# Kernel optimization log

Hardware: AMD Instinct MI355X
Metric: run time of the kernel (lower is better)

## Reference

```python
import jax, jax.numpy as jnp
import numpy as np

N = 50000      # nodes
E = 800000     # edges
D_IN = 128     # input feature dim
HID = 64       # out_channels (per-head dim; concat=False -> head mean)
HEADS = 2
NEG_SLOPE = 0.2


def gat_layer(x, src, dst, Ws, Wd, a_s, a_d, b):
    # PyG GATConv, add_self_loops=False, concat=False (mean over heads)
    n = x.shape[0]
    H, C = a_s.shape
    hs = (x @ Ws).reshape(n, H, C)          # source-side features [N,H,C]
    hd = (x @ Wd).reshape(n, H, C)          # dest-side features   [N,H,C]
    als = (hs * a_s).sum(-1)                # [N,H]
    ald = (hd * a_d).sum(-1)                # [N,H]
    e = jax.nn.leaky_relu(als[src] + ald[dst], NEG_SLOPE)   # [E,H]
    # segment softmax over edges grouped by destination node
    m = jax.ops.segment_max(e, dst, num_segments=n)
    m = jax.lax.stop_gradient(jnp.where(jnp.isfinite(m), m, 0.0))
    ex = jnp.exp(e - m[dst])
    den = jax.ops.segment_sum(ex, dst, num_segments=n)
    alpha = ex / (den[dst] + 1e-16)                          # [E,H]
    out = jax.ops.segment_sum(hs[src] * alpha[:, :, None], dst, num_segments=n)
    return out.mean(axis=1) + b             # [N,C]


def setup_inputs() -> dict:
    key = jax.random.key(0)
    ks = jax.random.split(key, 32)
    d = {}
    d["x"] = jax.random.normal(ks[0], (N, D_IN), jnp.float32)
    d["edge_index"] = jax.random.randint(ks[1], (2, E), 0, N, jnp.int32)
    dins = [D_IN, HID, HID]
    i = 2
    for l in range(1, 4):
        din = dins[l - 1]
        s = 1.0 / np.sqrt(din)
        d[f"Ws{l}"] = jax.random.normal(ks[i], (din, HEADS * HID), jnp.float32) * s; i += 1
        d[f"Wd{l}"] = jax.random.normal(ks[i], (din, HEADS * HID), jnp.float32) * s; i += 1
        d[f"as{l}"] = jax.random.normal(ks[i], (HEADS, HID), jnp.float32) * 0.1; i += 1
        d[f"ad{l}"] = jax.random.normal(ks[i], (HEADS, HID), jnp.float32) * 0.1; i += 1
        d[f"b{l}"] = jnp.zeros((HID,), jnp.float32)
        d[f"Wl{l}"] = jax.random.normal(ks[i], (din, HID), jnp.float32) * s; i += 1
        d[f"bl{l}"] = jnp.zeros((HID,), jnp.float32)
    return d


def reference(x, edge_index,
              Ws1, Wd1, as1, ad1, b1, Wl1, bl1,
              Ws2, Wd2, as2, ad2, b2, Wl2, bl2,
              Ws3, Wd3, as3, ad3, b3, Wl3, bl3):
    src, dst = edge_index[0], edge_index[1]
    h = jax.nn.relu(gat_layer(x, src, dst, Ws1, Wd1, as1, ad1, b1) + x @ Wl1 + bl1)
    h = jax.nn.relu(gat_layer(h, src, dst, Ws2, Wd2, as2, ad2, b2) + h @ Wl2 + bl2)
    h = jax.nn.relu(gat_layer(h, src, dst, Ws3, Wd3, as3, ad3, b3) + h @ Wl3 + bl3)
    return h
```

## Files before the change

### kernel.cpp

```cpp
#include <hip/hip_runtime.h>
#include <hip/hip_bf16.h>

#define NN 50000
#define NE 800000
#define SCAN_BS 1024
#define SCAN_NB ((NN + SCAN_BS - 1) / SCAN_BS)

typedef __attribute__((ext_vector_type(8))) __bf16 bf16x8;
typedef __attribute__((ext_vector_type(4))) float float4v;

__device__ __forceinline__ unsigned pack_bf2(float lo, float hi) {
    union { __bf16 b; unsigned short u; } a, c;
    a.b = (__bf16)lo; c.b = (__bf16)hi;
    return (unsigned)a.u | ((unsigned)c.u << 16);
}
__device__ __forceinline__ float2 unpack_bf2(unsigned v) {
    union { unsigned short u; __bf16 b; } lo, hi;
    lo.u = (unsigned short)(v & 0xffff); hi.u = (unsigned short)(v >> 16);
    return make_float2((float)lo.b, (float)hi.b);
}


__global__ void __launch_bounds__(256)
hist_kernel(const int* __restrict__ ei, int* __restrict__ deg, int* __restrict__ rank)
{
    int e = blockIdx.x * 256 + threadIdx.x;
    if (e >= NE) return;
    rank[e] = atomicAdd(&deg[ei[NE + e]], 1);
}

__global__ void __launch_bounds__(SCAN_BS)
scan1_kernel(const int* __restrict__ deg, int* __restrict__ exl, int* __restrict__ bsum)
{
    __shared__ int sh[SCAN_BS];
    int t = threadIdx.x;
    int i = blockIdx.x * SCAN_BS + t;
    int v = (i < NN) ? deg[i] : 0;
    sh[t] = v;
    __syncthreads();
    for (int off = 1; off < SCAN_BS; off <<= 1) {
        int u = (t >= off) ? sh[t - off] : 0;
        __syncthreads();
        sh[t] += u;
        __syncthreads();
    }
    if (i < NN) exl[i] = sh[t] - v;
    if (t == SCAN_BS - 1) bsum[blockIdx.x] = sh[t];
}

__global__ void __launch_bounds__(64)
scan2_kernel(const int* __restrict__ bsum, int* __restrict__ boff, int* __restrict__ row)
{
    int l = threadIdx.x;
    int v = (l < SCAN_NB) ? bsum[l] : 0;
    int own = v;
    for (int off = 1; off < 64; off <<= 1) {
        int u = __shfl_up(v, off);
        if (l >= off) v += u;
    }
    if (l < SCAN_NB) boff[l] = v - own;
    if (l == 63) row[NN] = v;
}

__global__ void __launch_bounds__(SCAN_BS)
scan3_kernel(const int* __restrict__ exl, const int* __restrict__ boff,
             int* __restrict__ row)
{
    int i = blockIdx.x * SCAN_BS + threadIdx.x;
    if (i >= NN) return;
    row[i] = exl[i] + boff[blockIdx.x];
}

__global__ void __launch_bounds__(256)
scatter_kernel(const int* __restrict__ ei, const int* __restrict__ rank,
               const int* __restrict__ row, int* __restrict__ csr_src)
{
    int e = blockIdx.x * 256 + threadIdx.x;
    if (e >= NE) return;
    int s = ei[e], d = ei[NE + e];
    int p = row[d] + rank[e];
    csr_src[p] = s;
}


__global__ void __launch_bounds__(256)
convert_x_kernel(const float* __restrict__ x, __bf16* __restrict__ xb, int n)
{
    int i = blockIdx.x * 256 + threadIdx.x;
    if (i < n) xb[i] = (__bf16)x[i];
}

template <int K>
__global__ void __launch_bounds__(256)
convert_w_kernel(const float* __restrict__ Ws, const float* __restrict__ Wd,
                 const float* __restrict__ Wl, __bf16* __restrict__ Wt)
{
    int i = blockIdx.x * 256 + threadIdx.x;
    if (i >= 320 * K) return;
    int c = i / K, k = i % K;
    float v;
    if (c < 128)      v = Ws[k * 128 + c];
    else if (c < 256) v = Wd[k * 128 + (c - 128)];
    else              v = Wl[k * 64 + (c - 256)];
    Wt[i] = (__bf16)v;
}

template <int K>
__global__ void __launch_bounds__(256)
mfma_gemm(const __bf16* __restrict__ xb, const __bf16* __restrict__ Wt,
          const float* __restrict__ a_s, const float* __restrict__ a_d,
          unsigned* __restrict__ hsb, float* __restrict__ lin,
          float* __restrict__ als, float* __restrict__ ald)
{
    __shared__ __align__(16) char ldsW[320 * 144];

    const int tid  = threadIdx.x;
    const int lane = tid & 63;
    const int wave = tid >> 6;
    const int l15 = lane & 15, quad = lane >> 4;
    const int n0 = blockIdx.x * 64 + wave * 16;
    const int nA = min(n0 + l15, NN - 1);

    bf16x8 afr[K / 32];
#pragma unroll
    for (int ks = 0; ks < K / 32; ++ks)
        afr[ks] = *(const bf16x8*)(xb + (size_t)nA * K + ks * 32 + quad * 8);

    float4v acc[20];
#pragma unroll
    for (int t = 0; t < 20; ++t) acc[t] = (float4v){0.f, 0.f, 0.f, 0.f};

#pragma unroll
    for (int h = 0; h < K / 64; ++h) {
        uint4 tmp[10];
#pragma unroll
        for (int i = 0; i < 10; ++i) {
            int idx = i * 256 + tid;
            int r = idx >> 3, c = idx & 7;
            tmp[i] = *(const uint4*)(Wt + (size_t)r * K + h * 64 + c * 8);
        }
        if (h) __syncthreads();
#pragma unroll
        for (int i = 0; i < 10; ++i) {
            int idx = i * 256 + tid;
            int r = idx >> 3, c = idx & 7;
            *(uint4*)&ldsW[r * 144 + c * 16] = tmp[i];
        }
        __syncthreads();

#pragma unroll
        for (int ksh = 0; ksh < 2; ++ksh) {
            int ks = h * 2 + ksh;
#pragma unroll
            for (int t = 0; t < 20; ++t) {
                bf16x8 bf = *(const bf16x8*)&ldsW[(t * 16 + l15) * 144 + (ksh * 4 + quad) * 16];
                acc[t] = __builtin_amdgcn_mfma_f32_16x16x32_bf16(afr[ks], bf, acc[t], 0, 0, 0);
            }
        }
    }

#pragma unroll
    for (int t = 0; t < 4; ++t) {
        int col = t * 16 + l15;
#pragma unroll
        for (int r = 0; r < 4; ++r) {
            int n = n0 + quad * 4 + r;
            if (n < NN) hsb[(size_t)n * 64 + col] = pack_bf2(acc[t][r], acc[t + 4][r]);
        }
    }
#pragma unroll
    for (int t = 16; t < 20; ++t) {
        int col = (t - 16) * 16 + l15;
#pragma unroll
        for (int r = 0; r < 4; ++r) {
            int n = n0 + quad * 4 + r;
            if (n < NN) lin[(size_t)n * 64 + col] = acc[t][r];
        }
    }

    float s0[4], s1[4], d0[4], d1[4];
#pragma unroll
    for (int r = 0; r < 4; ++r) { s0[r] = 0.f; s1[r] = 0.f; d0[r] = 0.f; d1[r] = 0.f; }
#pragma unroll
    for (int t = 0; t < 4; ++t) {
        float as0 = a_s[t * 16 + l15];
        float as1 = a_s[64 + t * 16 + l15];
        float ad0 = a_d[t * 16 + l15];
        float ad1 = a_d[64 + t * 16 + l15];
#pragma unroll
        for (int r = 0; r < 4; ++r) {
            s0[r] += acc[t][r] * as0;
            s1[r] += acc[t + 4][r] * as1;
            d0[r] += acc[t + 8][r] * ad0;
            d1[r] += acc[t + 12][r] * ad1;
        }
    }
#pragma unroll
    for (int m = 1; m < 16; m <<= 1) {
#pragma unroll
        for (int r = 0; r < 4; ++r) {
            s0[r] += __shfl_xor(s0[r], m);
            s1[r] += __shfl_xor(s1[r], m);
            d0[r] += __shfl_xor(d0[r], m);
            d1[r] += __shfl_xor(d1[r], m);
        }
    }
    if (l15 == 0) {
#pragma unroll
        for (int r = 0; r < 4; ++r) {
            int n = n0 + quad * 4 + r;
            if (n < NN) {
                als[n * 2 + 0] = s0[r];
                als[n * 2 + 1] = s1[r];
                ald[n * 2 + 0] = d0[r];
                ald[n * 2 + 1] = d1[r];
            }
        }
    }
}


__device__ __forceinline__ float2 edge_w(const float* __restrict__ als, int s,
                                         float ad0, float ad1)
{
    float2 al = *(const float2*)&als[s * 2];
    float e0 = al.x + ad0; e0 = (e0 >= 0.f) ? e0 : 0.2f * e0;
    float e1 = al.y + ad1; e1 = (e1 >= 0.f) ? e1 : 0.2f * e1;
    return make_float2(__expf(e0), __expf(e1));
}

__device__ __forceinline__ void store_q(float* p, float v0, float v1, float v2, float v3) {
    *(float4*)p = make_float4(v0, v1, v2, v3);
}
__device__ __forceinline__ void store_q(__bf16* p, float v0, float v1, float v2, float v3) {
    *(uint2*)p = make_uint2(pack_bf2(v0, v1), pack_bf2(v2, v3));
}

template <typename TO>
__global__ void __launch_bounds__(256)
gat_aggregate(const int* __restrict__ row, const int* __restrict__ csr_src,
              const float* __restrict__ als, const float* __restrict__ ald,
              const unsigned* __restrict__ hsb, const float* __restrict__ lin,
              const float* __restrict__ b, const float* __restrict__ bl,
              TO* __restrict__ out)
{
    int w = (blockIdx.x * 256 + threadIdx.x) >> 6;
    int lane = threadIdx.x & 63;
    int q = lane >> 4;
    int l15 = lane & 15;
    if (w >= NN) return;
    int p0 = row[w], p1 = row[w + 1];
    float ad0 = ald[w * 2 + 0];
    float ad1 = ald[w * 2 + 1];

    float a0[4] = {0.f, 0.f, 0.f, 0.f};
    float a1[4] = {0.f, 0.f, 0.f, 0.f};
    float den0 = 0.f, den1 = 0.f;

    int p = p0 + q;
    for (; p + 4 < p1; p += 8) {
        int sA = csr_src[p];
        int sB = csr_src[p + 4];
        float2 eA = edge_w(als, sA, ad0, ad1);
        float2 eB = edge_w(als, sB, ad0, ad1);
        uint4 gA = *(const uint4*)&hsb[(size_t)sA * 64 + 4 * l15];
        uint4 gB = *(const uint4*)&hsb[(size_t)sB * 64 + 4 * l15];
        den0 += eA.x + eB.x;
        den1 += eA.y + eB.y;
        float2 h;
        h = unpack_bf2(gA.x); a0[0] += eA.x * h.x; a1[0] += eA.y * h.y;
        h = unpack_bf2(gA.y); a0[1] += eA.x * h.x; a1[1] += eA.y * h.y;
        h = unpack_bf2(gA.z); a0[2] += eA.x * h.x; a1[2] += eA.y * h.y;
        h = unpack_bf2(gA.w); a0[3] += eA.x * h.x; a1[3] += eA.y * h.y;
        h = unpack_bf2(gB.x); a0[0] += eB.x * h.x; a1[0] += eB.y * h.y;
        h = unpack_bf2(gB.y); a0[1] += eB.x * h.x; a1[1] += eB.y * h.y;
        h = unpack_bf2(gB.z); a0[2] += eB.x * h.x; a1[2] += eB.y * h.y;
        h = unpack_bf2(gB.w); a0[3] += eB.x * h.x; a1[3] += eB.y * h.y;
    }
    for (; p < p1; p += 4) {
        int s = csr_src[p];
        float2 e = edge_w(als, s, ad0, ad1);
        uint4 g = *(const uint4*)&hsb[(size_t)s * 64 + 4 * l15];
        den0 += e.x; den1 += e.y;
        float2 h;
        h = unpack_bf2(g.x); a0[0] += e.x * h.x; a1[0] += e.y * h.y;
        h = unpack_bf2(g.y); a0[1] += e.x * h.x; a1[1] += e.y * h.y;
        h = unpack_bf2(g.z); a0[2] += e.x * h.x; a1[2] += e.y * h.y;
        h = unpack_bf2(g.w); a0[3] += e.x * h.x; a1[3] += e.y * h.y;
    }

#pragma unroll
    for (int i = 0; i < 4; ++i) {
        a0[i] += __shfl_xor(a0[i], 16); a0[i] += __shfl_xor(a0[i], 32);
        a1[i] += __shfl_xor(a1[i], 16); a1[i] += __shfl_xor(a1[i], 32);
    }
    den0 += __shfl_xor(den0, 16); den0 += __shfl_xor(den0, 32);
    den1 += __shfl_xor(den1, 16); den1 += __shfl_xor(den1, 32);

    if (q == 0) {
        int c0 = 4 * l15;
        float r0 = 1.f / (den0 + 1e-16f);
        float r1 = 1.f / (den1 + 1e-16f);
        float4 lv = *(const float4*)&lin[(size_t)w * 64 + c0];
        float v0 = 0.5f * (a0[0] * r0 + a1[0] * r1) + b[c0 + 0] + bl[c0 + 0] + lv.x;
        float v1 = 0.5f * (a0[1] * r0 + a1[1] * r1) + b[c0 + 1] + bl[c0 + 1] + lv.y;
        float v2 = 0.5f * (a0[2] * r0 + a1[2] * r1) + b[c0 + 2] + bl[c0 + 2] + lv.z;
        float v3 = 0.5f * (a0[3] * r0 + a1[3] * r1) + b[c0 + 3] + bl[c0 + 3] + lv.w;
        store_q(&out[(size_t)w * 64 + c0],
                fmaxf(v0, 0.f), fmaxf(v1, 0.f), fmaxf(v2, 0.f), fmaxf(v3, 0.f));
    }
}


extern "C" void kernel_launch(void* const* d_in, const int* in_sizes, int n_in,
                              void* d_out, int out_size, void* d_ws, size_t ws_size,
                              hipStream_t stream)
{
    const float* x  = (const float*)d_in[0];
    const int*   ei = (const int*)d_in[1];
    const float* Ws[3]; const float* Wd[3]; const float* As[3]; const float* Ad[3];
    const float* Bb[3]; const float* Wl[3]; const float* Bl[3];
    for (int l = 0; l < 3; ++l) {
        int base = 2 + 7 * l;
        Ws[l] = (const float*)d_in[base + 0];
        Wd[l] = (const float*)d_in[base + 1];
        As[l] = (const float*)d_in[base + 2];
        Ad[l] = (const float*)d_in[base + 3];
        Bb[l] = (const float*)d_in[base + 4];
        Wl[l] = (const float*)d_in[base + 5];
        Bl[l] = (const float*)d_in[base + 6];
    }

    float* ws = (float*)d_ws;
    unsigned* hsb = (unsigned*)ws;
    float* lin  = (float*)(hsb + (size_t)NN * 64);
    float* als  = lin + (size_t)NN * 64;
    float* ald  = als + (size_t)NN * 2;
    __bf16* xb  = (__bf16*)(ald + (size_t)NN * 2);
    __bf16* hb  = xb + (size_t)NN * 128;
    __bf16* Wt1 = hb + (size_t)NN * 64;
    __bf16* Wt2 = Wt1 + 320 * 128;
    __bf16* Wt3 = Wt2 + 320 * 64;
    int* row     = (int*)(Wt3 + 320 * 64);
    int* deg     = row + (NN + 1);
    int* rank    = deg + NN;
    int* exl     = rank + NE;
    int* bsum    = exl + NN;
    int* boff    = bsum + SCAN_NB;
    int* csr_src = boff + SCAN_NB;

    const int EB  = (NE + 255) / 256;
    const int WB  = (NN * 64 + 255) / 256;
    const int GB  = (NN + 63) / 64;

    hipMemsetAsync(deg, 0, sizeof(int) * NN, stream);
    hist_kernel<<<EB, 256, 0, stream>>>(ei, deg, rank);
    scan1_kernel<<<SCAN_NB, SCAN_BS, 0, stream>>>(deg, exl, bsum);
    scan2_kernel<<<1, 64, 0, stream>>>(bsum, boff, row);
    scan3_kernel<<<SCAN_NB, SCAN_BS, 0, stream>>>(exl, boff, row);
    scatter_kernel<<<EB, 256, 0, stream>>>(ei, rank, row, csr_src);

    convert_x_kernel<<<(NN * 128 + 255) / 256, 256, 0, stream>>>(x, xb, NN * 128);
    convert_w_kernel<128><<<(320 * 128 + 255) / 256, 256, 0, stream>>>(Ws[0], Wd[0], Wl[0], Wt1);
    convert_w_kernel<64><<<(320 * 64 + 255) / 256, 256, 0, stream>>>(Ws[1], Wd[1], Wl[1], Wt2);
    convert_w_kernel<64><<<(320 * 64 + 255) / 256, 256, 0, stream>>>(Ws[2], Wd[2], Wl[2], Wt3);

    for (int l = 0; l < 3; ++l) {
        if (l == 0) {
            mfma_gemm<128><<<GB, 256, 0, stream>>>(xb, Wt1, As[0], Ad[0], hsb, lin, als, ald);
        } else {
            const __bf16* wt = (l == 1) ? Wt2 : Wt3;
            mfma_gemm<64><<<GB, 256, 0, stream>>>(hb, wt, As[l], Ad[l], hsb, lin, als, ald);
        }
        if (l == 2) {
            gat_aggregate<float><<<WB, 256, 0, stream>>>(
                row, csr_src, als, ald, hsb, lin, Bb[l], Bl[l], (float*)d_out);
        } else {
            gat_aggregate<__bf16><<<WB, 256, 0, stream>>>(
                row, csr_src, als, ald, hsb, lin, Bb[l], Bl[l], hb);
        }
    }
}
```

Measured before the change: 372.8 us.

## Fuse weight conversion into histogram kernel, convert x in GEMM, unroll aggregation

Merges the three weight-conversion launches into the edge-histogram kernel as extra blocks. The separate fp32-to-bf16 conversion of x is dropped, and the layer-1 GEMM now loads fp32 x and converts it in registers. The aggregation edge loop gets a 4-way unrolled main loop ahead of the existing 2-way loop. Together these cut launches and one full write and read of x, and raise memory-level parallelism in the gather. The costs are a larger first-layer A load (fp32 instead of bf16) and higher register pressure in the aggregation kernel.

Measured after the change: 353.3 us. 5.2% less time.

```diff
diff --git a/kernel.cpp b/kernel.cpp
--- a/kernel.cpp
+++ b/kernel.cpp
@@ -5,6 +5,7 @@
 #define NE 800000
 #define SCAN_BS 1024
 #define SCAN_NB ((NN + SCAN_BS - 1) / SCAN_BS)
+#define EB ((NE + 255) / 256)
 
 typedef __attribute__((ext_vector_type(8))) __bf16 bf16x8;
 typedef __attribute__((ext_vector_type(4))) float float4v;
@@ -21,13 +22,42 @@
 }
 
 
+__device__ __forceinline__ void convert_w_part(const float* __restrict__ Ws,
+                                               const float* __restrict__ Wd,
+                                               const float* __restrict__ Wl,
+                                               __bf16* __restrict__ Wt, int K, int i)
+{
+    if (i >= 320 * K) return;
+    int c = i / K, k = i % K;
+    float v;
+    if (c < 128)      v = Ws[k * 128 + c];
+    else if (c < 256) v = Wd[k * 128 + (c - 128)];
+    else              v = Wl[k * 64 + (c - 256)];
+    Wt[i] = (__bf16)v;
+}
+
 __global__ void __launch_bounds__(256)
-hist_kernel(const int* __restrict__ ei, int* __restrict__ deg, int* __restrict__ rank)
-{
-    int e = blockIdx.x * 256 + threadIdx.x;
-    if (e >= NE) return;
-    rank[e] = atomicAdd(&deg[ei[NE + e]], 1);
-}
+prep_kernel(const int* __restrict__ ei, int* __restrict__ deg, int* __restrict__ rank,
+            const float* __restrict__ Ws1, const float* __restrict__ Wd1,
+            const float* __restrict__ Wl1, __bf16* __restrict__ Wt1,
+            const float* __restrict__ Ws2, const float* __restrict__ Wd2,
+            const float* __restrict__ Wl2, __bf16* __restrict__ Wt2,
+            const float* __restrict__ Ws3, const float* __restrict__ Wd3,
+            const float* __restrict__ Wl3, __bf16* __restrict__ Wt3)
+{
+    int bi = blockIdx.x;
+    if (bi < EB) {
+        int e = bi * 256 + threadIdx.x;
+        if (e < NE) rank[e] = atomicAdd(&deg[ei[NE + e]], 1);
+    } else if (bi < EB + 160) {
+        convert_w_part(Ws1, Wd1, Wl1, Wt1, 128, (bi - EB) * 256 + threadIdx.x);
+    } else if (bi < EB + 240) {
+        convert_w_part(Ws2, Wd2, Wl2, Wt2, 64, (bi - EB - 160) * 256 + threadIdx.x);
+    } else {
+        convert_w_part(Ws3, Wd3, Wl3, Wt3, 64, (bi - EB - 240) * 256 + threadIdx.x);
+    }
+}
+
 
 __global__ void __launch_bounds__(SCAN_BS)
 scan1_kernel(const int* __restrict__ deg, int* __restrict__ exl, int* __restrict__ bsum)
@@ -83,31 +113,19 @@
 }
 
 
+__device__ __forceinline__ bf16x8 load_af(const __bf16* p) { return *(const bf16x8*)p; }
+__device__ __forceinline__ bf16x8 load_af(const float* p) {
+    float4 u = *(const float4*)p;
+    float4 v = *(const float4*)(p + 4);
+    bf16x8 r;
+    r[0] = (__bf16)u.x; r[1] = (__bf16)u.y; r[2] = (__bf16)u.z; r[3] = (__bf16)u.w;
+    r[4] = (__bf16)v.x; r[5] = (__bf16)v.y; r[6] = (__bf16)v.z; r[7] = (__bf16)v.w;
+    return r;
+}
+
+template <int K, typename TIN>
 __global__ void __launch_bounds__(256)
-convert_x_kernel(const float* __restrict__ x, __bf16* __restrict__ xb, int n)
-{
-    int i = blockIdx.x * 256 + threadIdx.x;
-    if (i < n) xb[i] = (__bf16)x[i];
-}
-
-template <int K>
-__global__ void __launch_bounds__(256)
-convert_w_kernel(const float* __restrict__ Ws, const float* __restrict__ Wd,
-                 const float* __restrict__ Wl, __bf16* __restrict__ Wt)
-{
-    int i = blockIdx.x * 256 + threadIdx.x;
-    if (i >= 320 * K) return;
-    int c = i / K, k = i % K;
-    float v;
-    if (c < 128)      v = Ws[k * 128 + c];
-    else if (c < 256) v = Wd[k * 128 + (c - 128)];
-    else              v = Wl[k * 64 + (c - 256)];
-    Wt[i] = (__bf16)v;
-}
-
-template <int K>
-__global__ void __launch_bounds__(256)
-mfma_gemm(const __bf16* __restrict__ xb, const __bf16* __restrict__ Wt,
+mfma_gemm(const TIN* __restrict__ xin, const __bf16* __restrict__ Wt,
           const float* __restrict__ a_s, const float* __restrict__ a_d,
           unsigned* __restrict__ hsb, float* __restrict__ lin,
           float* __restrict__ als, float* __restrict__ ald)
@@ -124,7 +142,7 @@
     bf16x8 afr[K / 32];
 #pragma unroll
     for (int ks = 0; ks < K / 32; ++ks)
-        afr[ks] = *(const bf16x8*)(xb + (size_t)nA * K + ks * 32 + quad * 8);
+        afr[ks] = load_af(xin + (size_t)nA * K + ks * 32 + quad * 8);
 
     float4v acc[20];
 #pragma unroll
@@ -258,6 +276,39 @@
     float den0 = 0.f, den1 = 0.f;
 
     int p = p0 + q;
+    for (; p + 12 < p1; p += 16) {
+        int sA = csr_src[p];
+        int sB = csr_src[p + 4];
+        int sC = csr_src[p + 8];
+        int sD = csr_src[p + 12];
+        float2 eA = edge_w(als, sA, ad0, ad1);
+        float2 eB = edge_w(als, sB, ad0, ad1);
+        float2 eC = edge_w(als, sC, ad0, ad1);
+        float2 eD = edge_w(als, sD, ad0, ad1);
+        uint4 gA = *(const uint4*)&hsb[(size_t)sA * 64 + 4 * l15];
+        uint4 gB = *(const uint4*)&hsb[(size_t)sB * 64 + 4 * l15];
+        uint4 gC = *(const uint4*)&hsb[(size_t)sC * 64 + 4 * l15];
+        uint4 gD = *(const uint4*)&hsb[(size_t)sD * 64 + 4 * l15];
+        den0 += (eA.x + eB.x) + (eC.x + eD.x);
+        den1 += (eA.y + eB.y) + (eC.y + eD.y);
+        float2 h;
+        h = unpack_bf2(gA.x); a0[0] += eA.x * h.x; a1[0] += eA.y * h.y;
+        h = unpack_bf2(gA.y); a0[1] += eA.x * h.x; a1[1] += eA.y * h.y;
+        h = unpack_bf2(gA.z); a0[2] += eA.x * h.x; a1[2] += eA.y * h.y;
+        h = unpack_bf2(gA.w); a0[3] += eA.x * h.x; a1[3] += eA.y * h.y;
+        h = unpack_bf2(gB.x); a0[0] += eB.x * h.x; a1[0] += eB.y * h.y;
+        h = unpack_bf2(gB.y); a0[1] += eB.x * h.x; a1[1] += eB.y * h.y;
+        h = unpack_bf2(gB.z); a0[2] += eB.x * h.x; a1[2] += eB.y * h.y;
+        h = unpack_bf2(gB.w); a0[3] += eB.x * h.x; a1[3] += eB.y * h.y;
+        h = unpack_bf2(gC.x); a0[0] += eC.x * h.x; a1[0] += eC.y * h.y;
+        h = unpack_bf2(gC.y); a0[1] += eC.x * h.x; a1[1] += eC.y * h.y;
+        h = unpack_bf2(gC.z); a0[2] += eC.x * h.x; a1[2] += eC.y * h.y;
+        h = unpack_bf2(gC.w); a0[3] += eC.x * h.x; a1[3] += eC.y * h.y;
+        h = unpack_bf2(gD.x); a0[0] += eD.x * h.x; a1[0] += eD.y * h.y;
+        h = unpack_bf2(gD.y); a0[1] += eD.x * h.x; a1[1] += eD.y * h.y;
+        h = unpack_bf2(gD.z); a0[2] += eD.x * h.x; a1[2] += eD.y * h.y;
+        h = unpack_bf2(gD.w); a0[3] += eD.x * h.x; a1[3] += eD.y * h.y;
+    }
     for (; p + 4 < p1; p += 8) {
         int sA = csr_src[p];
         int sB = csr_src[p + 4];
@@ -336,8 +387,7 @@
     float* lin  = (float*)(hsb + (size_t)NN * 64);
     float* als  = lin + (size_t)NN * 64;
     float* ald  = als + (size_t)NN * 2;
-    __bf16* xb  = (__bf16*)(ald + (size_t)NN * 2);
-    __bf16* hb  = xb + (size_t)NN * 128;
+    __bf16* hb  = (__bf16*)(ald + (size_t)NN * 2);
     __bf16* Wt1 = hb + (size_t)NN * 64;
     __bf16* Wt2 = Wt1 + 320 * 128;
     __bf16* Wt3 = Wt2 + 320 * 64;
@@ -349,28 +399,27 @@
     int* boff    = bsum + SCAN_NB;
     int* csr_src = boff + SCAN_NB;
 
-    const int EB  = (NE + 255) / 256;
     const int WB  = (NN * 64 + 255) / 256;
     const int GB  = (NN + 63) / 64;
 
     hipMemsetAsync(deg, 0, sizeof(int) * NN, stream);
-    hist_kernel<<<EB, 256, 0, stream>>>(ei, deg, rank);
+    prep_kernel<<<EB + 320, 256, 0, stream>>>(ei, deg, rank,
+        Ws[0], Wd[0], Wl[0], Wt1,
+        Ws[1], Wd[1], Wl[1], Wt2,
+        Ws[2], Wd[2], Wl[2], Wt3);
     scan1_kernel<<<SCAN_NB, SCAN_BS, 0, stream>>>(deg, exl, bsum);
     scan2_kernel<<<1, 64, 0, stream>>>(bsum, boff, row);
     scan3_kernel<<<SCAN_NB, SCAN_BS, 0, stream>>>(exl, boff, row);
     scatter_kernel<<<EB, 256, 0, stream>>>(ei, rank, row, csr_src);
 
-    convert_x_kernel<<<(NN * 128 + 255) / 256, 256, 0, stream>>>(x, xb, NN * 128);
-    convert_w_kernel<128><<<(320 * 128 + 255) / 256, 256, 0, stream>>>(Ws[0], Wd[0], Wl[0], Wt1);
-    convert_w_kernel<64><<<(320 * 64 + 255) / 256, 256, 0, stream>>>(Ws[1], Wd[1], Wl[1], Wt2);
-    convert_w_kernel<64><<<(320 * 64 + 255) / 256, 256, 0, stream>>>(Ws[2], Wd[2], Wl[2], Wt3);
-
     for (int l = 0; l < 3; ++l) {
         if (l == 0) {
-            mfma_gemm<128><<<GB, 256, 0, stream>>>(xb, Wt1, As[0], Ad[0], hsb, lin, als, ald);
+            mfma_gemm<128, float><<<GB, 256, 0, stream>>>(
+                x, Wt1, As[0], Ad[0], hsb, lin, als, ald);
         } else {
             const __bf16* wt = (l == 1) ? Wt2 : Wt3;
-            mfma_gemm<64><<<GB, 256, 0, stream>>>(hb, wt, As[l], Ad[l], hsb, lin, als, ald);
+            mfma_gemm<64, __bf16><<<GB, 256, 0, stream>>>(
+                hb, wt, As[l], Ad[l], hsb, lin, als, ald);
         }
         if (l == 2) {
             gat_aggregate<float><<<WB, 256, 0, stream>>>(
```
